# Kernel optimization log

Hardware: AMD Instinct MI355X
Metric: run time of the kernel (lower is better)

Reference implementation:

```python
import jax, jax.numpy as jnp
import numpy as np

B, N, C = 4, 2048, 64   # batch, tokens, num_feat
HS = 512                # hidden_size
H = HS // C             # 8 heads, head_dim = C = 64
EPS = 1e-6


def _ln(x, g, b):
    m = x.mean(-1, keepdims=True)
    v = ((x - m) ** 2).mean(-1, keepdims=True)
    return (x - m) / jnp.sqrt(v + EPS) * g + b


def setup_inputs() -> dict:
    key = jax.random.key(0)
    ks = jax.random.split(key, 8)
    s = 0.02
    return {
        "x": jax.random.normal(ks[0], (B, N, C), jnp.float32),
        "g1": jnp.ones((C,), jnp.float32),
        "be1": jnp.zeros((C,), jnp.float32),
        "Wqkv": jax.random.normal(ks[1], (C, 3 * HS), jnp.float32) * s,
        "bqkv": jnp.zeros((3 * HS,), jnp.float32),
        "Wout": jax.random.normal(ks[2], (HS, C), jnp.float32) * s,
        "bout": jnp.zeros((C,), jnp.float32),
        "g2": jnp.ones((C,), jnp.float32),
        "be2": jnp.zeros((C,), jnp.float32),
        "W1": jax.random.normal(ks[3], (C, HS // 8), jnp.float32) * s,
        "b1": jax.random.normal(ks[4], (HS // 8,), jnp.float32) * 1e-6,
        "W2": jax.random.normal(ks[5], (HS // 8, C), jnp.float32) * s,
        "b2": jax.random.normal(ks[6], (C,), jnp.float32) * 1e-6,
    }


def reference(x, g1, be1, Wqkv, bqkv, Wout, bout, g2, be2, W1, b1, W2, b2):
    b_, n_, c_ = x.shape
    hs = Wout.shape[0]
    h_ = hs // c_
    res = x
    y = _ln(x, g1, be1)
    # fused QKV: (B,N,3*HS) -> (3,B,H,N,D) with D = c_
    qkv = (y @ Wqkv + bqkv).reshape(b_, n_, 3, h_, c_).transpose(2, 0, 3, 1, 4)
    q, k, v = qkv[0], qkv[1], qkv[2]
    scores = jnp.einsum('bhqd,bhkd->bhqk', q, k) / jnp.sqrt(jnp.asarray(c_, x.dtype))
    probs = jax.nn.softmax(scores, axis=-1)
    ctx = jnp.einsum('bhqk,bhkd->bhqd', probs, v)
    ctx = ctx.transpose(0, 2, 1, 3).reshape(b_, n_, hs)
    attn = jax.nn.gelu(ctx @ Wout + bout, approximate=False)  # GELU after out proj per source
    x2 = attn + res
    y2 = _ln(x2, g2, be2)
    mlp = jax.nn.gelu(y2 @ W1 + b1, approximate=False) @ W2 + b2
    return mlp + x2
```

## Files before the change

### kernel.cpp

```cpp
#include <hip/hip_runtime.h>


#define NN 2048
#define CC 64
#define HH 8
#define HSZ 512
#define QKSCALE 0.42466092f
#define LSTR 88

typedef __bf16 bf16x8 __attribute__((ext_vector_type(8)));
typedef float f32x4 __attribute__((ext_vector_type(4)));

__device__ __forceinline__ float b2f(unsigned short u) {
  union { unsigned int i; float f; } v; v.i = ((unsigned int)u) << 16; return v.f;
}
__device__ __forceinline__ unsigned short f2b(float f) {
  union { float f; unsigned int i; } v; v.f = f;
  unsigned int r = v.i + 0x7FFFu + ((v.i >> 16) & 1u);
  return (unsigned short)(r >> 16);
}
__device__ __forceinline__ unsigned int pk2(float a, float b) {
  return (unsigned int)f2b(a) | ((unsigned int)f2b(b) << 16);
}
__device__ __forceinline__ unsigned char f2fp8(float f) {
  int p = __builtin_amdgcn_cvt_pk_fp8_f32(f, f, 0, false);
  return (unsigned char)(p & 0xFF);
}
__device__ __forceinline__ float gelu_f(float x) {
  return 0.5f * x * (1.0f + erff(x * 0.7071067811865475f));
}

__global__ __launch_bounds__(256) void k_ln_qkv(
    const float* __restrict__ x,
    const float* __restrict__ g1,
    const float* __restrict__ be1,
    const float* __restrict__ W,
    const float* __restrict__ bqkv,
    unsigned char* __restrict__ Qb,
    unsigned char* __restrict__ Kb,
    unsigned char* __restrict__ VbT)
{
  __shared__ __align__(16) unsigned short As[64 * 72];
  __shared__ __align__(16) unsigned short Ws[128 * 72];
  unsigned char* Es = (unsigned char*)As;
  const int tid = threadIdx.x, wv = tid >> 6, lane = tid & 63;
  const int col = lane & 15, quad = lane >> 4;
  const int bm = blockIdx.x & 127, bn = blockIdx.x >> 7;
  const int m0 = bm * 64, nw = bn * 128;

  const int c4 = tid & 15;
  float4 gv = *(const float4*)(g1 + c4 * 4);
  float4 bv = *(const float4*)(be1 + c4 * 4);
  #pragma unroll
  for (int s = 0; s < 4; ++s) {
    int idx = s * 256 + tid;
    int row = idx >> 4;
    float4 xv = *(const float4*)(x + (size_t)(m0 + row) * CC + c4 * 4);
    float ps = xv.x + xv.y + xv.z + xv.w;
    float ps2 = xv.x * xv.x + xv.y * xv.y + xv.z * xv.z + xv.w * xv.w;
    #pragma unroll
    for (int off = 8; off; off >>= 1) {
      ps += __shfl_xor(ps, off, 16);
      ps2 += __shfl_xor(ps2, off, 16);
    }
    float mean = ps * (1.0f / 64.0f);
    float var = ps2 * (1.0f / 64.0f) - mean * mean;
    float rs = rsqrtf(var + 1e-6f);
    uint2 packed;
    packed.x = pk2((xv.x - mean) * rs * gv.x + bv.x, (xv.y - mean) * rs * gv.y + bv.y);
    packed.y = pk2((xv.z - mean) * rs * gv.z + bv.z, (xv.w - mean) * rs * gv.w + bv.w);
    *(uint2*)&As[row * 72 + c4 * 4] = packed;
  }

  {
    const int c_loc = tid & 127;
    const int kg = tid >> 7;
    const int ng = nw + c_loc;
    #pragma unroll
    for (int g = 0; g < 4; ++g) {
      float wv8[8];
      #pragma unroll
      for (int j = 0; j < 8; ++j) wv8[j] = W[(size_t)(kg * 32 + g * 8 + j) * 1536 + ng];
      uint4 u;
      u.x = pk2(wv8[0], wv8[1]); u.y = pk2(wv8[2], wv8[3]);
      u.z = pk2(wv8[4], wv8[5]); u.w = pk2(wv8[6], wv8[7]);
      *(uint4*)&Ws[c_loc * 72 + kg * 32 + g * 8] = u;
    }
  }
  __syncthreads();

  bf16x8 af0 = *(const bf16x8*)&As[(wv * 16 + col) * 72 + quad * 8];
  bf16x8 af1 = *(const bf16x8*)&As[(wv * 16 + col) * 72 + 32 + quad * 8];

  f32x4 acc[8];
  #pragma unroll
  for (int nt = 0; nt < 8; ++nt) acc[nt] = (f32x4){0.f, 0.f, 0.f, 0.f};
  #pragma unroll
  for (int nt = 0; nt < 8; ++nt) {
    bf16x8 b0 = *(const bf16x8*)&Ws[(nt * 16 + col) * 72 + quad * 8];
    bf16x8 b1 = *(const bf16x8*)&Ws[(nt * 16 + col) * 72 + 32 + quad * 8];
    acc[nt] = __builtin_amdgcn_mfma_f32_16x16x32_bf16(af0, b0, acc[nt], 0, 0, 0);
    acc[nt] = __builtin_amdgcn_mfma_f32_16x16x32_bf16(af1, b1, acc[nt], 0, 0, 0);
  }
  __syncthreads();

  const int bb = m0 >> 11;
  const int nloc = m0 & 2047;
  const int which = nw >> 9;
  const int hbase = (nw >> 6) & 7;
  const int tloc = wv * 16 + quad * 4;

  if (which == 2) {
    #pragma unroll
    for (int nt = 0; nt < 8; ++nt) {
      const int hb = nt >> 2, d0 = (nt & 3) * 16;
      const float bias = bqkv[nw + nt * 16 + col];
      int lo = __builtin_amdgcn_cvt_pk_fp8_f32(acc[nt][0] + bias, acc[nt][1] + bias, 0, false);
      int full = __builtin_amdgcn_cvt_pk_fp8_f32(acc[nt][2] + bias, acc[nt][3] + bias, lo, true);
      *(unsigned int*)&Es[hb * 4096 + (d0 + col) * 64 + tloc] = (unsigned int)full;
    }
    __syncthreads();
    const int d = tid >> 2, nseg = (tid & 3) * 16;
    #pragma unroll
    for (int hb = 0; hb < 2; ++hb) {
      size_t off = ((size_t)(bb * HH + hbase + hb) * CC + d) * NN + nloc + nseg;
      *(uint4*)(VbT + off) = *(const uint4*)&Es[hb * 4096 + tid * 16];
    }
  } else {
    const float scale = (which == 0) ? QKSCALE : 1.0f;
    #pragma unroll
    for (int nt = 0; nt < 8; ++nt) {
      const int hb = nt >> 2, d0 = (nt & 3) * 16;
      const float bias = bqkv[nw + nt * 16 + col];
      #pragma unroll
      for (int r = 0; r < 4; ++r)
        Es[hb * 4096 + (tloc + r) * 64 + d0 + col] = f2fp8((acc[nt][r] + bias) * scale);
    }
    __syncthreads();
    unsigned char* dst = (which == 0) ? Qb : Kb;
    #pragma unroll
    for (int hb = 0; hb < 2; ++hb) {
      size_t off = ((size_t)(bb * HH + hbase + hb) * NN + nloc) * CC + tid * 16;
      *(uint4*)(dst + off) = *(const uint4*)&Es[hb * 4096 + tid * 16];
    }
  }
}

__global__ __launch_bounds__(256) void k_attn(
    const unsigned char* __restrict__ Q,
    const unsigned char* __restrict__ K,
    const unsigned char* __restrict__ VT,
    const float* __restrict__ Wout,
    unsigned short* __restrict__ part,
    float* __restrict__ lsums)
{
  __shared__ __align__(16) unsigned char smem[27648];
  unsigned char* Ks = smem;
  unsigned char* Vt = smem + 5632;
  unsigned short* Wb = (unsigned short*)smem;
  unsigned short* Ob = (unsigned short*)(smem + 9216);
  const int tid = threadIdx.x, wv = tid >> 6, lane = tid & 63;
  const int col = lane & 15, quad = lane >> 4;
  const int bid = blockIdx.x;
  const int tc = bid & 1, qc = (bid >> 1) & 15, bh = bid >> 5;
  const size_t base = (size_t)bh * NN * CC;
  const int q0 = qc * 128 + wv * 32;
  const int t0 = tc * 1024;
  const int srow = tid >> 2, sc16 = (tid & 3) << 4;

  if (tid < 80) {
    unsigned int fill = (tid == 0) ? 0x38383838u : 0u;
    #pragma unroll
    for (int w8 = 0; w8 < 11; ++w8)
      *(unsigned int*)&Vt[(64 + (tid >> 0) % 16) * LSTR + 0] = 0u;
  }
  {
    int idx = tid * 8;
    if (idx < 16 * LSTR) {
      unsigned long long z = 0ull;
      *(unsigned long long*)&Vt[64 * LSTR + idx] = z;
    }
  }
  __syncthreads();
  if (tid < 11) *(unsigned int*)&Vt[64 * LSTR + tid * 4] = 0x38383838u;

  long qf[2][2];
  #pragma unroll
  for (int mt = 0; mt < 2; ++mt)
    #pragma unroll
    for (int kh = 0; kh < 2; ++kh)
      qf[mt][kh] = *(const long*)(Q + base + (size_t)(q0 + mt * 16 + col) * CC + kh * 32 + quad * 8);

  f32x4 o[2][4];
  f32x4 ol[2];
  #pragma unroll
  for (int mt = 0; mt < 2; ++mt) {
    #pragma unroll
    for (int dt = 0; dt < 4; ++dt) o[mt][dt] = (f32x4){0.f, 0.f, 0.f, 0.f};
    ol[mt] = (f32x4){0.f, 0.f, 0.f, 0.f};
  }
  const int sl0 = ((quad & 1) << 5) + col;
  const int sl1 = sl0 + 16;
  const bool hiq = (quad >= 2);

  for (int kt = 0; kt < 16; ++kt) {
    const int tb = t0 + kt * 64;
    {
      uint4 kv = *(const uint4*)(K + base + (size_t)(tb + srow) * CC + sc16);
      uint4 vv = *(const uint4*)(VT + base + (size_t)srow * NN + tb + sc16);
      *(uint2*)&Ks[srow * LSTR + sc16] = make_uint2(kv.x, kv.y);
      *(uint2*)&Ks[srow * LSTR + sc16 + 8] = make_uint2(kv.z, kv.w);
      *(uint2*)&Vt[srow * LSTR + sc16] = make_uint2(vv.x, vv.y);
      *(uint2*)&Vt[srow * LSTR + sc16 + 8] = make_uint2(vv.z, vv.w);
    }
    __syncthreads();

    unsigned int Dw[2][4];
    #pragma unroll
    for (int ct = 0; ct < 4; ++ct) {
      long k0 = *(const long*)&Ks[(ct * 16 + col) * LSTR + quad * 8];
      long k1 = *(const long*)&Ks[(ct * 16 + col) * LSTR + 32 + quad * 8];
      #pragma unroll
      for (int mt = 0; mt < 2; ++mt) {
        f32x4 a = (f32x4){0.f, 0.f, 0.f, 0.f};
        a = __builtin_amdgcn_mfma_f32_16x16x32_fp8_fp8(k0, qf[mt][0], a, 0, 0, 0);
        a = __builtin_amdgcn_mfma_f32_16x16x32_fp8_fp8(k1, qf[mt][1], a, 0, 0, 0);
        float p0 = __builtin_amdgcn_exp2f(a[0]);
        float p1 = __builtin_amdgcn_exp2f(a[1]);
        float p2 = __builtin_amdgcn_exp2f(a[2]);
        float p3 = __builtin_amdgcn_exp2f(a[3]);
        int lo = __builtin_amdgcn_cvt_pk_fp8_f32(p0, p1, 0, false);
        Dw[mt][ct] = (unsigned int)__builtin_amdgcn_cvt_pk_fp8_f32(p2, p3, lo, true);
      }
    }

    #pragma unroll
    for (int kh = 0; kh < 2; ++kh) {
      long pb[2];
      #pragma unroll
      for (int mt = 0; mt < 2; ++mt) {
        unsigned int a0 = (unsigned int)__shfl((int)Dw[mt][2 * kh], sl0, 64);
        unsigned int b0 = (unsigned int)__shfl((int)Dw[mt][2 * kh + 1], sl0, 64);
        unsigned int a1 = (unsigned int)__shfl((int)Dw[mt][2 * kh], sl1, 64);
        unsigned int b1 = (unsigned int)__shfl((int)Dw[mt][2 * kh + 1], sl1, 64);
        unsigned long lo = hiq ? b0 : a0;
        unsigned long hi = hiq ? b1 : a1;
        pb[mt] = (long)(lo | (hi << 32));
      }
      #pragma unroll
      for (int dt = 0; dt < 4; ++dt) {
        long vf = *(const long*)&Vt[(dt * 16 + col) * LSTR + kh * 32 + quad * 8];
        o[0][dt] = __builtin_amdgcn_mfma_f32_16x16x32_fp8_fp8(vf, pb[0], o[0][dt], 0, 0, 0);
        o[1][dt] = __builtin_amdgcn_mfma_f32_16x16x32_fp8_fp8(vf, pb[1], o[1][dt], 0, 0, 0);
      }
      long vl = *(const long*)&Vt[(64 + col) * LSTR + kh * 32 + quad * 8];
      ol[0] = __builtin_amdgcn_mfma_f32_16x16x32_fp8_fp8(vl, pb[0], ol[0], 0, 0, 0);
      ol[1] = __builtin_amdgcn_mfma_f32_16x16x32_fp8_fp8(vl, pb[1], ol[1], 0, 0, 0);
    }
    __syncthreads();
  }

  const int h = bh & 7, b = bh >> 3;
  #pragma unroll
  for (int mt = 0; mt < 2; ++mt) {
    if (quad == 0)
      lsums[(size_t)(tc * 32 + bh) * NN + q0 + mt * 16 + col] = ol[mt][0];
  }

  {
    const int c = tid & 63, kg = tid >> 6;
    #pragma unroll
    for (int j = 0; j < 16; ++j)
      Wb[c * 72 + kg * 16 + j] = f2b(Wout[(size_t)(h * 64 + kg * 16 + j) * 64 + c]);
  }
  unsigned short* Obw = Ob + wv * (32 * 72);
  #pragma unroll
  for (int mt = 0; mt < 2; ++mt)
    #pragma unroll
    for (int dt = 0; dt < 4; ++dt) {
      uint2 u;
      u.x = pk2(o[mt][dt][0], o[mt][dt][1]);
      u.y = pk2(o[mt][dt][2], o[mt][dt][3]);
      *(uint2*)&Obw[(mt * 16 + col) * 72 + dt * 16 + quad * 4] = u;
    }
  __syncthreads();

  #pragma unroll
  for (int mt = 0; mt < 2; ++mt) {
    bf16x8 oa0 = *(const bf16x8*)&Obw[(mt * 16 + col) * 72 + quad * 8];
    bf16x8 oa1 = *(const bf16x8*)&Obw[(mt * 16 + col) * 72 + 32 + quad * 8];
    #pragma unroll
    for (int nt = 0; nt < 4; ++nt) {
      bf16x8 bw0 = *(const bf16x8*)&Wb[(nt * 16 + col) * 72 + quad * 8];
      bf16x8 bw1 = *(const bf16x8*)&Wb[(nt * 16 + col) * 72 + 32 + quad * 8];
      f32x4 ac = (f32x4){0.f, 0.f, 0.f, 0.f};
      ac = __builtin_amdgcn_mfma_f32_16x16x32_bf16(oa0, bw0, ac, 0, 0, 0);
      ac = __builtin_amdgcn_mfma_f32_16x16x32_bf16(oa1, bw1, ac, 0, 0, 0);
      #pragma unroll
      for (int r = 0; r < 4; ++r) {
        int n = q0 + mt * 16 + quad * 4 + r;
        part[((size_t)(tc * 32 + bh) * NN + n) * CC + nt * 16 + col] = f2b(ac[r]);
      }
    }
  }
}

__global__ __launch_bounds__(256) void k_post(
    const unsigned short* __restrict__ part,
    const float* __restrict__ lsums,
    const float* __restrict__ x,
    const float* __restrict__ bout,
    const float* __restrict__ g2,
    const float* __restrict__ be2,
    const float* __restrict__ W1,
    const float* __restrict__ b1,
    const float* __restrict__ W2,
    const float* __restrict__ b2v,
    float* __restrict__ out)
{
  __shared__ __align__(16) unsigned short Ws1[64 * 64];
  __shared__ __align__(16) unsigned short Ws2[64 * 64];
  __shared__ float ys[8][64], hs[8][64];
  const int tid = threadIdx.x, wid = tid >> 6, lane = tid & 63;
  const int w2 = wid * 2;
  const int tk0 = blockIdx.x * 8 + w2;

  #pragma unroll
  for (int p = 0; p < 4; ++p) {
    int idx = p * 256 + tid;
    float4 a1 = *(const float4*)(W1 + idx * 4);
    float4 a2 = *(const float4*)(W2 + idx * 4);
    uint2 u1; u1.x = pk2(a1.x, a1.y); u1.y = pk2(a1.z, a1.w);
    uint2 u2; u2.x = pk2(a2.x, a2.y); u2.y = pk2(a2.z, a2.w);
    *(uint2*)&Ws1[idx * 4] = u1;
    *(uint2*)&Ws2[idx * 4] = u2;
  }

  const float boutl = bout[lane];
  const float g2l = g2[lane], be2l = be2[lane];
  float x2v[2];
  #pragma unroll
  for (int t = 0; t < 2; ++t) {
    const int tk = tk0 + t;
    const int b = tk >> 11, n = tk & 2047;
    float proj = 0.f;
    #pragma unroll
    for (int h = 0; h < 8; ++h) {
      size_t i0 = (size_t)(b * HH + h) * NN + n;
      size_t i1 = i0 + (size_t)32 * NN;
      float p = b2f(part[i0 * CC + lane]) + b2f(part[i1 * CC + lane]);
      float l = lsums[i0] + lsums[i1];
      proj += p * __builtin_amdgcn_rcpf(l);
    }
    float a = gelu_f(proj + boutl);
    float x2 = a + x[(size_t)tk * CC + lane];
    x2v[t] = x2;
    float s = x2;
    #pragma unroll
    for (int off = 32; off; off >>= 1) s += __shfl_xor(s, off, 64);
    float mean = s * (1.0f / 64.0f);
    float d = x2 - mean;
    float vs = d * d;
    #pragma unroll
    for (int off = 32; off; off >>= 1) vs += __shfl_xor(vs, off, 64);
    float var = vs * (1.0f / 64.0f);
    ys[w2 + t][lane] = d * rsqrtf(var + 1e-6f) * g2l + be2l;
  }
  __syncthreads();

  float acc2[2] = {0.f, 0.f};
  #pragma unroll 8
  for (int c = 0; c < 64; ++c) {
    float w = b2f(Ws1[c * 64 + lane]);
    acc2[0] += ys[w2][c] * w;
    acc2[1] += ys[w2 + 1][c] * w;
  }
  const float b1l = b1[lane];
  hs[w2][lane] = gelu_f(acc2[0] + b1l);
  hs[w2 + 1][lane] = gelu_f(acc2[1] + b1l);

  float acc3[2] = {0.f, 0.f};
  #pragma unroll 8
  for (int c = 0; c < 64; ++c) {
    float w = b2f(Ws2[c * 64 + lane]);
    acc3[0] += hs[w2][c] * w;
    acc3[1] += hs[w2 + 1][c] * w;
  }
  const float b2l = b2v[lane];
  #pragma unroll
  for (int t = 0; t < 2; ++t)
    out[(size_t)(tk0 + t) * CC + lane] = acc3[t] + b2l + x2v[t];
}

extern "C" void kernel_launch(void* const* d_in, const int* in_sizes, int n_in,
                              void* d_out, int out_size, void* d_ws, size_t ws_size,
                              hipStream_t stream) {
  const float* x    = (const float*)d_in[0];
  const float* g1   = (const float*)d_in[1];
  const float* be1  = (const float*)d_in[2];
  const float* Wqkv = (const float*)d_in[3];
  const float* bqkv = (const float*)d_in[4];
  const float* Wout = (const float*)d_in[5];
  const float* bout = (const float*)d_in[6];
  const float* g2   = (const float*)d_in[7];
  const float* be2  = (const float*)d_in[8];
  const float* W1   = (const float*)d_in[9];
  const float* b1   = (const float*)d_in[10];
  const float* W2   = (const float*)d_in[11];
  const float* b2   = (const float*)d_in[12];
  float* out = (float*)d_out;

  unsigned char* wsb = (unsigned char*)d_ws;
  const size_t SZ = (size_t)4 * HH * NN * CC;
  unsigned char* Qb   = wsb;
  unsigned char* Kb   = wsb + SZ;
  unsigned char* VbT  = wsb + 2 * SZ;
  unsigned short* part = (unsigned short*)(wsb + 3 * SZ);
  float* lsums         = (float*)(wsb + 3 * SZ + 4 * SZ);

  k_ln_qkv<<<1536, 256, 0, stream>>>(x, g1, be1, Wqkv, bqkv, Qb, Kb, VbT);
  k_attn<<<1024, 256, 0, stream>>>(Qb, Kb, VbT, Wout, part, lsums);
  k_post<<<1024, 256, 0, stream>>>(part, lsums, x, bout, g2, be2, W1, b1, W2, b2, out);
}
```

Measured before the change: 147.3 us.

## Double row tile in QKV projection and key tile in attention loop

The LN+QKV kernel now processes 128 rows per block instead of 64, so each converted bf16 weight tile is reused across two M subtiles and the grid is halved. The attention kernel now stages 128 keys per iteration instead of 64, with a wider V-transpose stride, which halves the number of loop iterations and block barriers. In exchange, register use (accumulators, Dw) and shared memory use per block grow, which may reduce occupancy.

```diff
diff --git a/kernel.cpp b/kernel.cpp
--- a/kernel.cpp
+++ b/kernel.cpp
@@ -6,7 +6,8 @@
 #define HH 8
 #define HSZ 512
 #define QKSCALE 0.42466092f
-#define LSTR 88
+#define KSTR 88
+#define VSTR 152
 
 typedef __bf16 bf16x8 __attribute__((ext_vector_type(8)));
 typedef float f32x4 __attribute__((ext_vector_type(4)));
@@ -40,22 +41,22 @@
     unsigned char* __restrict__ Kb,
     unsigned char* __restrict__ VbT)
 {
-  __shared__ __align__(16) unsigned short As[64 * 72];
+  __shared__ __align__(16) unsigned short As[128 * 72];
   __shared__ __align__(16) unsigned short Ws[128 * 72];
   unsigned char* Es = (unsigned char*)As;
   const int tid = threadIdx.x, wv = tid >> 6, lane = tid & 63;
   const int col = lane & 15, quad = lane >> 4;
-  const int bm = blockIdx.x & 127, bn = blockIdx.x >> 7;
-  const int m0 = bm * 64, nw = bn * 128;
+  const int bm = blockIdx.x & 63, bn = blockIdx.x >> 6;
+  const int m0b = bm * 128, nw = bn * 128;
 
   const int c4 = tid & 15;
   float4 gv = *(const float4*)(g1 + c4 * 4);
   float4 bv = *(const float4*)(be1 + c4 * 4);
   #pragma unroll
-  for (int s = 0; s < 4; ++s) {
+  for (int s = 0; s < 8; ++s) {
     int idx = s * 256 + tid;
     int row = idx >> 4;
-    float4 xv = *(const float4*)(x + (size_t)(m0 + row) * CC + c4 * 4);
+    float4 xv = *(const float4*)(x + (size_t)(m0b + row) * CC + c4 * 4);
     float ps = xv.x + xv.y + xv.z + xv.w;
     float ps2 = xv.x * xv.x + xv.y * xv.y + xv.z * xv.z + xv.w * xv.w;
     #pragma unroll
@@ -89,59 +90,79 @@
   }
   __syncthreads();
 
-  bf16x8 af0 = *(const bf16x8*)&As[(wv * 16 + col) * 72 + quad * 8];
-  bf16x8 af1 = *(const bf16x8*)&As[(wv * 16 + col) * 72 + 32 + quad * 8];
-
-  f32x4 acc[8];
-  #pragma unroll
-  for (int nt = 0; nt < 8; ++nt) acc[nt] = (f32x4){0.f, 0.f, 0.f, 0.f};
+  bf16x8 af[2][2];
+  #pragma unroll
+  for (int mt = 0; mt < 2; ++mt)
+    #pragma unroll
+    for (int h = 0; h < 2; ++h)
+      af[mt][h] = *(const bf16x8*)&As[(mt * 64 + wv * 16 + col) * 72 + h * 32 + quad * 8];
+
+  f32x4 acc[2][8];
+  #pragma unroll
+  for (int mt = 0; mt < 2; ++mt)
+    #pragma unroll
+    for (int nt = 0; nt < 8; ++nt) acc[mt][nt] = (f32x4){0.f, 0.f, 0.f, 0.f};
   #pragma unroll
   for (int nt = 0; nt < 8; ++nt) {
     bf16x8 b0 = *(const bf16x8*)&Ws[(nt * 16 + col) * 72 + quad * 8];
     bf16x8 b1 = *(const bf16x8*)&Ws[(nt * 16 + col) * 72 + 32 + quad * 8];
-    acc[nt] = __builtin_amdgcn_mfma_f32_16x16x32_bf16(af0, b0, acc[nt], 0, 0, 0);
-    acc[nt] = __builtin_amdgcn_mfma_f32_16x16x32_bf16(af1, b1, acc[nt], 0, 0, 0);
-  }
-  __syncthreads();
-
-  const int bb = m0 >> 11;
-  const int nloc = m0 & 2047;
+    #pragma unroll
+    for (int mt = 0; mt < 2; ++mt) {
+      acc[mt][nt] = __builtin_amdgcn_mfma_f32_16x16x32_bf16(af[mt][0], b0, acc[mt][nt], 0, 0, 0);
+      acc[mt][nt] = __builtin_amdgcn_mfma_f32_16x16x32_bf16(af[mt][1], b1, acc[mt][nt], 0, 0, 0);
+    }
+  }
+  __syncthreads();
+
   const int which = nw >> 9;
   const int hbase = (nw >> 6) & 7;
   const int tloc = wv * 16 + quad * 4;
 
-  if (which == 2) {
-    #pragma unroll
-    for (int nt = 0; nt < 8; ++nt) {
-      const int hb = nt >> 2, d0 = (nt & 3) * 16;
-      const float bias = bqkv[nw + nt * 16 + col];
-      int lo = __builtin_amdgcn_cvt_pk_fp8_f32(acc[nt][0] + bias, acc[nt][1] + bias, 0, false);
-      int full = __builtin_amdgcn_cvt_pk_fp8_f32(acc[nt][2] + bias, acc[nt][3] + bias, lo, true);
-      *(unsigned int*)&Es[hb * 4096 + (d0 + col) * 64 + tloc] = (unsigned int)full;
-    }
-    __syncthreads();
-    const int d = tid >> 2, nseg = (tid & 3) * 16;
-    #pragma unroll
-    for (int hb = 0; hb < 2; ++hb) {
-      size_t off = ((size_t)(bb * HH + hbase + hb) * CC + d) * NN + nloc + nseg;
-      *(uint4*)(VbT + off) = *(const uint4*)&Es[hb * 4096 + tid * 16];
-    }
-  } else {
-    const float scale = (which == 0) ? QKSCALE : 1.0f;
-    #pragma unroll
-    for (int nt = 0; nt < 8; ++nt) {
-      const int hb = nt >> 2, d0 = (nt & 3) * 16;
-      const float bias = bqkv[nw + nt * 16 + col];
-      #pragma unroll
-      for (int r = 0; r < 4; ++r)
-        Es[hb * 4096 + (tloc + r) * 64 + d0 + col] = f2fp8((acc[nt][r] + bias) * scale);
-    }
-    __syncthreads();
-    unsigned char* dst = (which == 0) ? Qb : Kb;
-    #pragma unroll
-    for (int hb = 0; hb < 2; ++hb) {
-      size_t off = ((size_t)(bb * HH + hbase + hb) * NN + nloc) * CC + tid * 16;
-      *(uint4*)(dst + off) = *(const uint4*)&Es[hb * 4096 + tid * 16];
+  #pragma unroll
+  for (int mt = 0; mt < 2; ++mt) {
+    unsigned char* Em = Es + mt * 8192;
+    if (which == 2) {
+      #pragma unroll
+      for (int nt = 0; nt < 8; ++nt) {
+        const int hb = nt >> 2, d0 = (nt & 3) * 16;
+        const float bias = bqkv[nw + nt * 16 + col];
+        int lo = __builtin_amdgcn_cvt_pk_fp8_f32(acc[mt][nt][0] + bias, acc[mt][nt][1] + bias, 0, false);
+        int full = __builtin_amdgcn_cvt_pk_fp8_f32(acc[mt][nt][2] + bias, acc[mt][nt][3] + bias, lo, true);
+        *(unsigned int*)&Em[hb * 4096 + (d0 + col) * 64 + tloc] = (unsigned int)full;
+      }
+    } else {
+      const float scale = (which == 0) ? QKSCALE : 1.0f;
+      #pragma unroll
+      for (int nt = 0; nt < 8; ++nt) {
+        const int hb = nt >> 2, d0 = (nt & 3) * 16;
+        const float bias = bqkv[nw + nt * 16 + col];
+        #pragma unroll
+        for (int r = 0; r < 4; ++r)
+          Em[hb * 4096 + (tloc + r) * 64 + d0 + col] = f2fp8((acc[mt][nt][r] + bias) * scale);
+      }
+    }
+  }
+  __syncthreads();
+
+  #pragma unroll
+  for (int mt = 0; mt < 2; ++mt) {
+    const int m0 = m0b + mt * 64;
+    const int bb = m0 >> 11;
+    const int nloc = m0 & 2047;
+    if (which == 2) {
+      const int d = tid >> 2, nseg = (tid & 3) * 16;
+      #pragma unroll
+      for (int hb = 0; hb < 2; ++hb) {
+        size_t off = ((size_t)(bb * HH + hbase + hb) * CC + d) * NN + nloc + nseg;
+        *(uint4*)(VbT + off) = *(const uint4*)&Es[mt * 8192 + hb * 4096 + tid * 16];
+      }
+    } else {
+      unsigned char* dst = (which == 0) ? Qb : Kb;
+      #pragma unroll
+      for (int hb = 0; hb < 2; ++hb) {
+        size_t off = ((size_t)(bb * HH + hbase + hb) * NN + nloc) * CC + tid * 16;
+        *(uint4*)(dst + off) = *(const uint4*)&Es[mt * 8192 + hb * 4096 + tid * 16];
+      }
     }
   }
 }
@@ -156,7 +177,7 @@
 {
   __shared__ __align__(16) unsigned char smem[27648];
   unsigned char* Ks = smem;
-  unsigned char* Vt = smem + 5632;
+  unsigned char* Vt = smem + 11264;
   unsigned short* Wb = (unsigned short*)smem;
   unsigned short* Ob = (unsigned short*)(smem + 9216);
   const int tid = threadIdx.x, wv = tid >> 6, lane = tid & 63;
@@ -166,23 +187,16 @@
   const size_t base = (size_t)bh * NN * CC;
   const int q0 = qc * 128 + wv * 32;
   const int t0 = tc * 1024;
-  const int srow = tid >> 2, sc16 = (tid & 3) << 4;
-
-  if (tid < 80) {
-    unsigned int fill = (tid == 0) ? 0x38383838u : 0u;
-    #pragma unroll
-    for (int w8 = 0; w8 < 11; ++w8)
-      *(unsigned int*)&Vt[(64 + (tid >> 0) % 16) * LSTR + 0] = 0u;
-  }
+
   {
-    int idx = tid * 8;
-    if (idx < 16 * LSTR) {
-      unsigned long long z = 0ull;
-      *(unsigned long long*)&Vt[64 * LSTR + idx] = z;
-    }
-  }
-  __syncthreads();
-  if (tid < 11) *(unsigned int*)&Vt[64 * LSTR + tid * 4] = 0x38383838u;
+    int idx = tid * 16;
+    if (idx < 16 * VSTR) {
+      uint4 z; z.x = 0; z.y = 0; z.z = 0; z.w = 0;
+      *(uint4*)&Vt[64 * VSTR + idx] = z;
+    }
+  }
+  __syncthreads();
+  if (tid < 32) *(unsigned int*)&Vt[64 * VSTR + tid * 4] = 0x38383838u;
 
   long qf[2][2];
   #pragma unroll
@@ -203,23 +217,33 @@
   const int sl1 = sl0 + 16;
   const bool hiq = (quad >= 2);
 
-  for (int kt = 0; kt < 16; ++kt) {
-    const int tb = t0 + kt * 64;
+  const int krow = tid >> 1, kc32 = (tid & 1) * 32;
+  const int vd = tid >> 3, voff = (tid & 7) * 16;
+
+  for (int kt = 0; kt < 8; ++kt) {
+    const int tb = t0 + kt * 128;
     {
-      uint4 kv = *(const uint4*)(K + base + (size_t)(tb + srow) * CC + sc16);
-      uint4 vv = *(const uint4*)(VT + base + (size_t)srow * NN + tb + sc16);
-      *(uint2*)&Ks[srow * LSTR + sc16] = make_uint2(kv.x, kv.y);
-      *(uint2*)&Ks[srow * LSTR + sc16 + 8] = make_uint2(kv.z, kv.w);
-      *(uint2*)&Vt[srow * LSTR + sc16] = make_uint2(vv.x, vv.y);
-      *(uint2*)&Vt[srow * LSTR + sc16 + 8] = make_uint2(vv.z, vv.w);
+      uint4 ka = *(const uint4*)(K + base + (size_t)(tb + krow) * CC + kc32);
+      uint4 kb2 = *(const uint4*)(K + base + (size_t)(tb + krow) * CC + kc32 + 16);
+      *(uint2*)&Ks[krow * KSTR + kc32] = make_uint2(ka.x, ka.y);
+      *(uint2*)&Ks[krow * KSTR + kc32 + 8] = make_uint2(ka.z, ka.w);
+      *(uint2*)&Ks[krow * KSTR + kc32 + 16] = make_uint2(kb2.x, kb2.y);
+      *(uint2*)&Ks[krow * KSTR + kc32 + 24] = make_uint2(kb2.z, kb2.w);
+      #pragma unroll
+      for (int p = 0; p < 2; ++p) {
+        int d = p * 32 + vd;
+        uint4 vv = *(const uint4*)(VT + base + (size_t)d * NN + tb + voff);
+        *(uint2*)&Vt[d * VSTR + voff] = make_uint2(vv.x, vv.y);
+        *(uint2*)&Vt[d * VSTR + voff + 8] = make_uint2(vv.z, vv.w);
+      }
     }
     __syncthreads();
 
-    unsigned int Dw[2][4];
-    #pragma unroll
-    for (int ct = 0; ct < 4; ++ct) {
-      long k0 = *(const long*)&Ks[(ct * 16 + col) * LSTR + quad * 8];
-      long k1 = *(const long*)&Ks[(ct * 16 + col) * LSTR + 32 + quad * 8];
+    unsigned int Dw[2][8];
+    #pragma unroll
+    for (int ct = 0; ct < 8; ++ct) {
+      long k0 = *(const long*)&Ks[(ct * 16 + col) * KSTR + quad * 8];
+      long k1 = *(const long*)&Ks[(ct * 16 + col) * KSTR + 32 + quad * 8];
       #pragma unroll
       for (int mt = 0; mt < 2; ++mt) {
         f32x4 a = (f32x4){0.f, 0.f, 0.f, 0.f};
@@ -235,7 +259,7 @@
     }
 
     #pragma unroll
-    for (int kh = 0; kh < 2; ++kh) {
+    for (int kh = 0; kh < 4; ++kh) {
       long pb[2];
       #pragma unroll
       for (int mt = 0; mt < 2; ++mt) {
@@ -249,11 +273,11 @@
       }
       #pragma unroll
       for (int dt = 0; dt < 4; ++dt) {
-        long vf = *(const long*)&Vt[(dt * 16 + col) * LSTR + kh * 32 + quad * 8];
+        long vf = *(const long*)&Vt[(dt * 16 + col) * VSTR + kh * 32 + quad * 8];
         o[0][dt] = __builtin_amdgcn_mfma_f32_16x16x32_fp8_fp8(vf, pb[0], o[0][dt], 0, 0, 0);
         o[1][dt] = __builtin_amdgcn_mfma_f32_16x16x32_fp8_fp8(vf, pb[1], o[1][dt], 0, 0, 0);
       }
-      long vl = *(const long*)&Vt[(64 + col) * LSTR + kh * 32 + quad * 8];
+      long vl = *(const long*)&Vt[(64 + col) * VSTR + kh * 32 + quad * 8];
       ol[0] = __builtin_amdgcn_mfma_f32_16x16x32_fp8_fp8(vl, pb[0], ol[0], 0, 0, 0);
       ol[1] = __builtin_amdgcn_mfma_f32_16x16x32_fp8_fp8(vl, pb[1], ol[1], 0, 0, 0);
     }
@@ -418,7 +442,7 @@
   unsigned short* part = (unsigned short*)(wsb + 3 * SZ);
   float* lsums         = (float*)(wsb + 3 * SZ + 4 * SZ);
 
-  k_ln_qkv<<<1536, 256, 0, stream>>>(x, g1, be1, Wqkv, bqkv, Qb, Kb, VbT);
+  k_ln_qkv<<<768, 256, 0, stream>>>(x, g1, be1, Wqkv, bqkv, Qb, Kb, VbT);
   k_attn<<<1024, 256, 0, stream>>>(Qb, Kb, VbT, Wout, part, lsums);
   k_post<<<1024, 256, 0, stream>>>(part, lsums, x, bout, g2, be2, W1, b1, W2, b2, out);
 }
```

Result: slower. 155.5 us (+5.6%).

## Split attention keys four ways, sum probs in registers, store partials as fp8

Applied to the files above, without the earlier changes.

Raises the key-split factor from 2 to 4 and doubles the attention grid, so each block handles 512 keys instead of 1024. The row-sum MFMA against a constant-filled V row is replaced by a register accumulation of the exp values plus a cross-lane shuffle reduction. Partial out-projection results are now stored as fp8 instead of bf16, and the output staging buffer is reused per m-tile to shrink shared memory. The post kernel now reads four fp8 partials and four lsums per head, which costs more reads and fp8 precision in exchange for more parallelism and fewer MFMAs.

```diff
diff --git a/kernel.cpp b/kernel.cpp
--- a/kernel.cpp
+++ b/kernel.cpp
@@ -25,6 +25,15 @@
 __device__ __forceinline__ unsigned char f2fp8(float f) {
   int p = __builtin_amdgcn_cvt_pk_fp8_f32(f, f, 0, false);
   return (unsigned char)(p & 0xFF);
+}
+__device__ __forceinline__ float fp8tof(unsigned char u) {
+#if __has_builtin(__builtin_amdgcn_cvt_f32_fp8)
+  return __builtin_amdgcn_cvt_f32_fp8((int)u, 0);
+#else
+  int e = (u >> 3) & 15, m = u & 7;
+  float v = e ? ldexpf((float)(8 + m), e - 10) : ldexpf((float)m, -9);
+  return (u & 0x80) ? -v : v;
+#endif
 }
 __device__ __forceinline__ float gelu_f(float x) {
   return 0.5f * x * (1.0f + erff(x * 0.7071067811865475f));
@@ -151,10 +160,10 @@
     const unsigned char* __restrict__ K,
     const unsigned char* __restrict__ VT,
     const float* __restrict__ Wout,
-    unsigned short* __restrict__ part,
+    unsigned char* __restrict__ part,
     float* __restrict__ lsums)
 {
-  __shared__ __align__(16) unsigned char smem[27648];
+  __shared__ __align__(16) unsigned char smem[18432];
   unsigned char* Ks = smem;
   unsigned char* Vt = smem + 5632;
   unsigned short* Wb = (unsigned short*)smem;
@@ -162,27 +171,11 @@
   const int tid = threadIdx.x, wv = tid >> 6, lane = tid & 63;
   const int col = lane & 15, quad = lane >> 4;
   const int bid = blockIdx.x;
-  const int tc = bid & 1, qc = (bid >> 1) & 15, bh = bid >> 5;
+  const int tc = bid & 3, qc = (bid >> 2) & 15, bh = bid >> 6;
   const size_t base = (size_t)bh * NN * CC;
   const int q0 = qc * 128 + wv * 32;
-  const int t0 = tc * 1024;
+  const int t0 = tc * 512;
   const int srow = tid >> 2, sc16 = (tid & 3) << 4;
-
-  if (tid < 80) {
-    unsigned int fill = (tid == 0) ? 0x38383838u : 0u;
-    #pragma unroll
-    for (int w8 = 0; w8 < 11; ++w8)
-      *(unsigned int*)&Vt[(64 + (tid >> 0) % 16) * LSTR + 0] = 0u;
-  }
-  {
-    int idx = tid * 8;
-    if (idx < 16 * LSTR) {
-      unsigned long long z = 0ull;
-      *(unsigned long long*)&Vt[64 * LSTR + idx] = z;
-    }
-  }
-  __syncthreads();
-  if (tid < 11) *(unsigned int*)&Vt[64 * LSTR + tid * 4] = 0x38383838u;
 
   long qf[2][2];
   #pragma unroll
@@ -192,18 +185,16 @@
       qf[mt][kh] = *(const long*)(Q + base + (size_t)(q0 + mt * 16 + col) * CC + kh * 32 + quad * 8);
 
   f32x4 o[2][4];
-  f32x4 ol[2];
-  #pragma unroll
-  for (int mt = 0; mt < 2; ++mt) {
+  float ls[2] = {0.f, 0.f};
+  #pragma unroll
+  for (int mt = 0; mt < 2; ++mt)
     #pragma unroll
     for (int dt = 0; dt < 4; ++dt) o[mt][dt] = (f32x4){0.f, 0.f, 0.f, 0.f};
-    ol[mt] = (f32x4){0.f, 0.f, 0.f, 0.f};
-  }
   const int sl0 = ((quad & 1) << 5) + col;
   const int sl1 = sl0 + 16;
   const bool hiq = (quad >= 2);
 
-  for (int kt = 0; kt < 16; ++kt) {
+  for (int kt = 0; kt < 8; ++kt) {
     const int tb = t0 + kt * 64;
     {
       uint4 kv = *(const uint4*)(K + base + (size_t)(tb + srow) * CC + sc16);
@@ -229,6 +220,7 @@
         float p1 = __builtin_amdgcn_exp2f(a[1]);
         float p2 = __builtin_amdgcn_exp2f(a[2]);
         float p3 = __builtin_amdgcn_exp2f(a[3]);
+        ls[mt] += (p0 + p1) + (p2 + p3);
         int lo = __builtin_amdgcn_cvt_pk_fp8_f32(p0, p1, 0, false);
         Dw[mt][ct] = (unsigned int)__builtin_amdgcn_cvt_pk_fp8_f32(p2, p3, lo, true);
       }
@@ -253,9 +245,6 @@
         o[0][dt] = __builtin_amdgcn_mfma_f32_16x16x32_fp8_fp8(vf, pb[0], o[0][dt], 0, 0, 0);
         o[1][dt] = __builtin_amdgcn_mfma_f32_16x16x32_fp8_fp8(vf, pb[1], o[1][dt], 0, 0, 0);
       }
-      long vl = *(const long*)&Vt[(64 + col) * LSTR + kh * 32 + quad * 8];
-      ol[0] = __builtin_amdgcn_mfma_f32_16x16x32_fp8_fp8(vl, pb[0], ol[0], 0, 0, 0);
-      ol[1] = __builtin_amdgcn_mfma_f32_16x16x32_fp8_fp8(vl, pb[1], ol[1], 0, 0, 0);
     }
     __syncthreads();
   }
@@ -263,8 +252,11 @@
   const int h = bh & 7, b = bh >> 3;
   #pragma unroll
   for (int mt = 0; mt < 2; ++mt) {
+    float v = ls[mt];
+    v += __shfl_xor(v, 16, 64);
+    v += __shfl_xor(v, 32, 64);
     if (quad == 0)
-      lsums[(size_t)(tc * 32 + bh) * NN + q0 + mt * 16 + col] = ol[mt][0];
+      lsums[(size_t)(tc * 32 + bh) * NN + q0 + mt * 16 + col] = v;
   }
 
   {
@@ -273,22 +265,20 @@
     for (int j = 0; j < 16; ++j)
       Wb[c * 72 + kg * 16 + j] = f2b(Wout[(size_t)(h * 64 + kg * 16 + j) * 64 + c]);
   }
-  unsigned short* Obw = Ob + wv * (32 * 72);
-  #pragma unroll
-  for (int mt = 0; mt < 2; ++mt)
+  __syncthreads();
+
+  unsigned short* Obw = Ob + wv * (16 * 72);
+  #pragma unroll
+  for (int mt = 0; mt < 2; ++mt) {
     #pragma unroll
     for (int dt = 0; dt < 4; ++dt) {
       uint2 u;
       u.x = pk2(o[mt][dt][0], o[mt][dt][1]);
       u.y = pk2(o[mt][dt][2], o[mt][dt][3]);
-      *(uint2*)&Obw[(mt * 16 + col) * 72 + dt * 16 + quad * 4] = u;
-    }
-  __syncthreads();
-
-  #pragma unroll
-  for (int mt = 0; mt < 2; ++mt) {
-    bf16x8 oa0 = *(const bf16x8*)&Obw[(mt * 16 + col) * 72 + quad * 8];
-    bf16x8 oa1 = *(const bf16x8*)&Obw[(mt * 16 + col) * 72 + 32 + quad * 8];
+      *(uint2*)&Obw[col * 72 + dt * 16 + quad * 4] = u;
+    }
+    bf16x8 oa0 = *(const bf16x8*)&Obw[col * 72 + quad * 8];
+    bf16x8 oa1 = *(const bf16x8*)&Obw[col * 72 + 32 + quad * 8];
     #pragma unroll
     for (int nt = 0; nt < 4; ++nt) {
       bf16x8 bw0 = *(const bf16x8*)&Wb[(nt * 16 + col) * 72 + quad * 8];
@@ -299,14 +289,14 @@
       #pragma unroll
       for (int r = 0; r < 4; ++r) {
         int n = q0 + mt * 16 + quad * 4 + r;
-        part[((size_t)(tc * 32 + bh) * NN + n) * CC + nt * 16 + col] = f2b(ac[r]);
+        part[((size_t)(tc * 32 + bh) * NN + n) * CC + nt * 16 + col] = f2fp8(ac[r]);
       }
     }
   }
 }
 
 __global__ __launch_bounds__(256) void k_post(
-    const unsigned short* __restrict__ part,
+    const unsigned char* __restrict__ part,
     const float* __restrict__ lsums,
     const float* __restrict__ x,
     const float* __restrict__ bout,
@@ -346,10 +336,13 @@
     float proj = 0.f;
     #pragma unroll
     for (int h = 0; h < 8; ++h) {
-      size_t i0 = (size_t)(b * HH + h) * NN + n;
-      size_t i1 = i0 + (size_t)32 * NN;
-      float p = b2f(part[i0 * CC + lane]) + b2f(part[i1 * CC + lane]);
-      float l = lsums[i0] + lsums[i1];
+      float p = 0.f, l = 0.f;
+      #pragma unroll
+      for (int c = 0; c < 4; ++c) {
+        size_t i = (size_t)(c * 32 + b * HH + h) * NN + n;
+        p += fp8tof(part[i * CC + lane]);
+        l += lsums[i];
+      }
       proj += p * __builtin_amdgcn_rcpf(l);
     }
     float a = gelu_f(proj + boutl);
@@ -415,10 +408,10 @@
   unsigned char* Qb   = wsb;
   unsigned char* Kb   = wsb + SZ;
   unsigned char* VbT  = wsb + 2 * SZ;
-  unsigned short* part = (unsigned short*)(wsb + 3 * SZ);
-  float* lsums         = (float*)(wsb + 3 * SZ + 4 * SZ);
+  unsigned char* part = wsb + 3 * SZ;
+  float* lsums        = (float*)(wsb + 3 * SZ + 4 * SZ);
 
   k_ln_qkv<<<1536, 256, 0, stream>>>(x, g1, be1, Wqkv, bqkv, Qb, Kb, VbT);
-  k_attn<<<1024, 256, 0, stream>>>(Qb, Kb, VbT, Wout, part, lsums);
+  k_attn<<<2048, 256, 0, stream>>>(Qb, Kb, VbT, Wout, part, lsums);
   k_post<<<1024, 256, 0, stream>>>(part, lsums, x, bout, g2, be2, W1, b1, W2, b2, out);
 }
```

Result: slower. 158.8 us (+7.8%).
